# Optimization experiments

Measured on AMD Instinct MI355X. Metric: run time of the kernel, lower is better.

Reference implementation:

```python
import jax, jax.numpy as jnp
import numpy as np

B, S, ENC, DEC, ATT = 32, 2048, 1024, 1024, 1024


def setup_inputs() -> dict:
    key = jax.random.key(0)
    k1, k2, k3, k4, k5, k6 = jax.random.split(key, 6)
    sc = lambda fan_in: 1.0 / np.sqrt(fan_in)
    return {
        "encoder_hidden_states": jax.random.normal(k1, (B, S, ENC), dtype=jnp.float32),
        "decoder_hidden_state": jax.random.normal(k2, (B, 1, DEC), dtype=jnp.float32),
        # nn.Linear stores weight as [out, in]; we keep [in, out] for x @ W
        "U_a": jax.random.uniform(k3, (ENC, ATT), jnp.float32, -sc(ENC), sc(ENC)),
        "W_a": jax.random.uniform(k4, (DEC, ATT), jnp.float32, -sc(DEC), sc(DEC)),
        "v_t": jax.random.uniform(k5, (ATT, 1), jnp.float32, -sc(ATT), sc(ATT)),
        "ffn": jax.random.uniform(k6, (ENC + DEC, DEC), jnp.float32, -sc(ENC + DEC), sc(ENC + DEC)),
    }


def reference(encoder_hidden_states, decoder_hidden_state, U_a, W_a, v_t, ffn):
    # additive (Bahdanau) attention
    u = jnp.einsum('bse,ea->bsa', encoder_hidden_states, U_a)      # [B,S,A]
    w = jnp.einsum('bqd,da->bqa', decoder_hidden_state, W_a)       # [B,1,A]
    e = jnp.tanh(w + u) @ v_t                                      # [B,S,1]
    align = jax.nn.softmax(e, axis=1)                              # softmax over seq
    # context = alignment^T @ encoder_states  -> [B,1,E]
    context = jnp.einsum('bsq,bse->bqe', align, encoder_hidden_states)
    cat = jnp.concatenate([decoder_hidden_state, context], axis=-1)  # [B,1,D+E]
    output = jnp.tanh(cat @ ffn)                                     # [B,1,D]
    return (output, context)
```

## Files before the change

kernel.cpp:

```cpp
#include <hip/hip_runtime.h>
#include <hip/hip_bf16.h>
#include <cstdint>
#include <cstddef>

#define B_  32
#define S_  2048
#define E_  1024
#define A_  1024
#define D_  1024
#define M_TOT (B_ * S_)

typedef __attribute__((ext_vector_type(8))) __bf16 bf16x8;
typedef __attribute__((ext_vector_type(4))) float  f32x4;

__device__ __forceinline__ float fast_tanh(float x) {
    float cx = fminf(fmaxf(x, -15.f), 15.f);
    float e2 = __expf(2.f * cx);
    return 1.f - 2.f / (e2 + 1.f);
}

__device__ __forceinline__ bf16x8 pack8(float4 f0, float4 f1) {
    bf16x8 r;
    r[0] = (__bf16)f0.x; r[1] = (__bf16)f0.y; r[2] = (__bf16)f0.z; r[3] = (__bf16)f0.w;
    r[4] = (__bf16)f1.x; r[5] = (__bf16)f1.y; r[6] = (__bf16)f1.z; r[7] = (__bf16)f1.w;
    return r;
}

typedef __attribute__((address_space(3))) uint32_t lds_u32_t;
typedef __attribute__((address_space(1))) const uint32_t gbl_u32_t;
__device__ __forceinline__ void async_ld16(const void* g, void* l) {
    __builtin_amdgcn_global_load_lds((gbl_u32_t*)g,
                                     (lds_u32_t*)(uint32_t)(uintptr_t)l,
                                     16, 0, 0);
}

__global__ __launch_bounds__(256) void k_cvt(const float* __restrict__ enc,
                                             __bf16* __restrict__ encB) {
    size_t base = (size_t)blockIdx.x * 8192 + (size_t)threadIdx.x * 8;
    #pragma unroll
    for (int it = 0; it < 4; ++it) {
        size_t idx = base + (size_t)it * 2048;
        float4 f0 = *(const float4*)(enc + idx);
        float4 f1 = *(const float4*)(enc + idx + 4);
        *(bf16x8*)(encB + idx) = pack8(f0, f1);
    }
}

__global__ __launch_bounds__(256) void k_trans_U(const float* __restrict__ Ua,
                                                 __bf16* __restrict__ Ut) {
    __shared__ float tile[64][65];
    int bid = blockIdx.x;
    int k0 = (bid >> 4) * 64, n0 = (bid & 15) * 64;
    int t = threadIdx.x;
    int r = t >> 6, c = t & 63;
    #pragma unroll
    for (int i = 0; i < 16; ++i)
        tile[i * 4 + r][c] = Ua[(size_t)(k0 + i * 4 + r) * 1024 + n0 + c];
    __syncthreads();
    #pragma unroll
    for (int i = 0; i < 16; ++i)
        Ut[(size_t)(n0 + i * 4 + r) * 1024 + k0 + c] = (__bf16)tile[c][i * 4 + r];
}

__global__ __launch_bounds__(256) void k_w_part(const float* __restrict__ dec,
                                                const float* __restrict__ Wa,
                                                float* __restrict__ w_part) {
    int bid = blockIdx.x;
    int ac = bid & 3, b = (bid >> 2) & 31, kc = bid >> 7;
    int a = ac * 256 + threadIdx.x;
    int k0 = kc * 128;
    float acc = 0.f;
    #pragma unroll 8
    for (int k = 0; k < 128; ++k)
        acc += dec[b * 1024 + k0 + k] * Wa[(size_t)(k0 + k) * 1024 + a];
    w_part[kc * 32768 + b * 1024 + a] = acc;
}

template<bool ASYNC_A>
__global__ __launch_bounds__(256) void k_gemm_e(
        const float* __restrict__ enc, const __bf16* __restrict__ encB,
        const __bf16* __restrict__ Ut,
        const float* __restrict__ w_part, const float* __restrict__ v,
        float* __restrict__ e_part) {
    __shared__ __bf16 lX[2][128 * 32];
    __shared__ __bf16 lU[2][128 * 32];
    __shared__ float  e_lds[2][128];

    const int t = threadIdx.x;
    const int bid = blockIdx.x;
    const int xcd = bid & 7;
    const int j_  = bid >> 3;
    const int m_tile = xcd * 64 + (j_ >> 3);
    const int n_tile = j_ & 7;
    const int m0 = m_tile * 128;
    const int n0 = n_tile * 128;
    const int wave = t >> 6;
    const int lane = t & 63;
    const int q = lane >> 4;
    const int c = lane & 15;
    const int wm = (wave >> 1) * 64;
    const int wn = (wave & 1) * 64;

    f32x4 acc[4][4];
    #pragma unroll
    for (int i = 0; i < 4; ++i)
        #pragma unroll
        for (int j = 0; j < 4; ++j)
            #pragma unroll
            for (int r = 0; r < 4; ++r) acc[i][j][r] = 0.f;

    const int lrow = lane >> 2;
    const int p    = lane & 3;
    const int sw   = (lrow >> 1) & 3;
    const int lcolS = ((p ^ sw)) * 8;

    const int xrow = wave * 32;

    const float*  gxa = enc  + (size_t)(m0 + xrow + lrow) * 1024 + lcolS;
    const __bf16* gxb = encB + (size_t)(m0 + xrow + lrow) * 1024 + lcolS;
    const __bf16* gub = Ut   + (size_t)(n0 + xrow + lrow) * 1024 + lcolS;

    float4 f0, f1, f2, f3;
    auto loadA = [&](int kk) {
        const float* pp = gxa + kk;
        f0 = *(const float4*)pp;
        f1 = *(const float4*)(pp + 4);
        f2 = *(const float4*)(pp + 16 * 1024);
        f3 = *(const float4*)(pp + 16 * 1024 + 4);
    };
    auto writeA = [&](int bsel) {
        *(bf16x8*)(&lX[bsel][(xrow + lrow) * 32 + p * 8])      = pack8(f0, f1);
        *(bf16x8*)(&lX[bsel][(xrow + 16 + lrow) * 32 + p * 8]) = pack8(f2, f3);
    };
    auto stageA = [&](int kk, int bsel) {
        async_ld16(gxb + kk,             &lX[bsel][xrow * 32]);
        async_ld16(gxb + kk + 16 * 1024, &lX[bsel][(xrow + 16) * 32]);
    };
    auto stageB = [&](int kk, int bsel) {
        async_ld16(gub + kk,             &lU[bsel][xrow * 32]);
        async_ld16(gub + kk + 16 * 1024, &lU[bsel][(xrow + 16) * 32]);
    };

    const int fcol = (q ^ ((c >> 1) & 3)) * 8;
    auto compute = [&](int bsel) {
        bf16x8 af[4], bfr[4];
        #pragma unroll
        for (int i = 0; i < 4; ++i)
            af[i] = *(const bf16x8*)(&lX[bsel][(wm + i * 16 + c) * 32 + fcol]);
        #pragma unroll
        for (int j = 0; j < 4; ++j)
            bfr[j] = *(const bf16x8*)(&lU[bsel][(wn + j * 16 + c) * 32 + fcol]);
        #pragma unroll
        for (int i = 0; i < 4; ++i)
            #pragma unroll
            for (int j = 0; j < 4; ++j)
                acc[i][j] = __builtin_amdgcn_mfma_f32_16x16x32_bf16(af[i], bfr[j], acc[i][j], 0, 0, 0);
    };

    if constexpr (ASYNC_A) {
        stageA(0, 0); stageB(0, 0);
        __syncthreads();
        for (int kk = 0; kk < 1024; kk += 64) {
            if (kk + 32 < 1024) { stageA(kk + 32, 1); stageB(kk + 32, 1); }
            compute(0);
            __syncthreads();
            if (kk + 64 < 1024) { stageA(kk + 64, 0); stageB(kk + 64, 0); }
            compute(1);
            __syncthreads();
        }
    } else {
        loadA(0);
        stageB(0, 0);
        writeA(0);
        __syncthreads();
        for (int kk = 0; kk < 1024; kk += 64) {
            if (kk + 32 < 1024) { loadA(kk + 32); stageB(kk + 32, 1); }
            compute(0);
            if (kk + 32 < 1024) writeA(1);
            __syncthreads();
            if (kk + 64 < 1024) { loadA(kk + 64); stageB(kk + 64, 0); }
            compute(1);
            if (kk + 64 < 1024) writeA(0);
            __syncthreads();
        }
    }

    const int b_idx = m0 >> 11;
    float wv[4], vv[4];
    #pragma unroll
    for (int j = 0; j < 4; ++j) {
        int col = n0 + wn + j * 16 + c;
        float s = 0.f;
        #pragma unroll
        for (int pp = 0; pp < 8; ++pp) s += w_part[pp * 32768 + b_idx * 1024 + col];
        wv[j] = s;
        vv[j] = v[col];
    }
    #pragma unroll
    for (int i = 0; i < 4; ++i) {
        float s0 = 0.f, s1 = 0.f, s2 = 0.f, s3 = 0.f;
        #pragma unroll
        for (int j = 0; j < 4; ++j) {
            s0 += fast_tanh(wv[j] + acc[i][j][0]) * vv[j];
            s1 += fast_tanh(wv[j] + acc[i][j][1]) * vv[j];
            s2 += fast_tanh(wv[j] + acc[i][j][2]) * vv[j];
            s3 += fast_tanh(wv[j] + acc[i][j][3]) * vv[j];
        }
        #pragma unroll
        for (int off = 1; off < 16; off <<= 1) {
            s0 += __shfl_xor(s0, off, 16);
            s1 += __shfl_xor(s1, off, 16);
            s2 += __shfl_xor(s2, off, 16);
            s3 += __shfl_xor(s3, off, 16);
        }
        if (c == 0) {
            int row = wm + i * 16 + q * 4;
            e_lds[wave & 1][row + 0] = s0;
            e_lds[wave & 1][row + 1] = s1;
            e_lds[wave & 1][row + 2] = s2;
            e_lds[wave & 1][row + 3] = s3;
        }
    }
    __syncthreads();
    if (t < 128)
        e_part[(size_t)n_tile * M_TOT + m0 + t] = e_lds[0][t] + e_lds[1][t];
}

__global__ __launch_bounds__(256) void k_softmax(const float* __restrict__ ep,
                                                 float* __restrict__ al) {
    int b = blockIdx.x, t = threadIdx.x;
    float ev[8];
    #pragma unroll
    for (int i = 0; i < 8; ++i) {
        int s = i * 256 + t;
        float x = 0.f;
        #pragma unroll
        for (int p = 0; p < 8; ++p) x += ep[p * M_TOT + b * 2048 + s];
        ev[i] = x;
    }
    float mx = ev[0];
    #pragma unroll
    for (int i = 1; i < 8; ++i) mx = fmaxf(mx, ev[i]);
    #pragma unroll
    for (int off = 1; off < 64; off <<= 1) mx = fmaxf(mx, __shfl_xor(mx, off, 64));
    __shared__ float redm[4];
    if ((t & 63) == 0) redm[t >> 6] = mx;
    __syncthreads();
    mx = fmaxf(fmaxf(redm[0], redm[1]), fmaxf(redm[2], redm[3]));

    float ex[8], sm = 0.f;
    #pragma unroll
    for (int i = 0; i < 8; ++i) { ex[i] = __expf(ev[i] - mx); sm += ex[i]; }
    #pragma unroll
    for (int off = 1; off < 64; off <<= 1) sm += __shfl_xor(sm, off, 64);
    __shared__ float reds[4];
    if ((t & 63) == 0) reds[t >> 6] = sm;
    __syncthreads();
    sm = reds[0] + reds[1] + reds[2] + reds[3];
    float inv = 1.f / sm;
    #pragma unroll
    for (int i = 0; i < 8; ++i) al[b * 2048 + i * 256 + t] = ex[i] * inv;
}

__global__ __launch_bounds__(256) void k_ctx(const float* __restrict__ enc,
                                             const float* __restrict__ al,
                                             float* __restrict__ ctx_part) {
    int b  = blockIdx.x >> 5;
    int sc = blockIdx.x & 31;
    int t  = threadIdx.x;
    int e4 = t * 4;
    float ax = 0.f, ay = 0.f, az = 0.f, aw = 0.f;
    int sbase = sc * 64;
    for (int i = 0; i < 64; i += 4) {
        #pragma unroll
        for (int u = 0; u < 4; ++u) {
            int s = sbase + i + u;
            float a = al[b * 2048 + s];
            float4 x = *(const float4*)(enc + (size_t)(b * 2048 + s) * 1024 + e4);
            ax += a * x.x; ay += a * x.y; az += a * x.z; aw += a * x.w;
        }
    }
    float4 r; r.x = ax; r.y = ay; r.z = az; r.w = aw;
    *(float4*)(ctx_part + ((size_t)sc * 32 + b) * 1024 + e4) = r;
}

__global__ __launch_bounds__(256) void k_final(const float* __restrict__ dec,
                                               const float* __restrict__ ffn,
                                               const float* __restrict__ ctx_part,
                                               float* __restrict__ out) {
    int b  = blockIdx.x >> 4;
    int dc = blockIdx.x & 15;
    int t  = threadIdx.x;
    __shared__ float cat[2048];
    __shared__ float red[4][64];

    #pragma unroll
    for (int r = 0; r < 4; ++r) {
        int e = r * 256 + t;
        cat[e] = dec[b * 1024 + e];
        float s = 0.f;
        #pragma unroll
        for (int p = 0; p < 32; ++p) s += ctx_part[((size_t)p * 32 + b) * 1024 + e];
        cat[1024 + e] = s;
        if (dc == 0) out[32768 + b * 1024 + e] = s;
    }
    __syncthreads();

    int dl = t & 63, ic = t >> 6;
    int d  = dc * 64 + dl;
    float acc = 0.f;
    int i0 = ic * 512;
    for (int i = 0; i < 512; i += 4) {
        float4 cv = *(const float4*)(cat + i0 + i);
        const float* fr = ffn + (size_t)(i0 + i) * 1024 + d;
        acc += cv.x * fr[0];
        acc += cv.y * fr[1024];
        acc += cv.z * fr[2048];
        acc += cv.w * fr[3072];
    }
    red[ic][dl] = acc;
    __syncthreads();
    if (t < 64) {
        float s = red[0][t] + red[1][t] + red[2][t] + red[3][t];
        out[b * 1024 + dc * 64 + t] = fast_tanh(s);
    }
}

extern "C" void kernel_launch(void* const* d_in, const int* in_sizes, int n_in,
                              void* d_out, int out_size, void* d_ws, size_t ws_size,
                              hipStream_t stream) {
    const float* enc = (const float*)d_in[0];
    const float* dec = (const float*)d_in[1];
    const float* Ua  = (const float*)d_in[2];
    const float* Wa  = (const float*)d_in[3];
    const float* vt  = (const float*)d_in[4];
    const float* ffn = (const float*)d_in[5];
    float* out = (float*)d_out;

    char* ws = (char*)d_ws;
    size_t off = 0;
    __bf16* Ut       = (__bf16*)(ws + off); off += (size_t)A_ * E_ * 2;
    float*  e_part   = (float*)(ws + off);  off += (size_t)8 * M_TOT * 4;
    float*  al       = (float*)(ws + off);  off += (size_t)M_TOT * 4;
    float*  w_part   = (float*)(ws + off);  off += (size_t)8 * B_ * 1024 * 4;
    float*  ctx_part = (float*)(ws + off);  off += (size_t)32 * B_ * 1024 * 4;
    __bf16* encB     = (__bf16*)(ws + off); off += (size_t)M_TOT * E_ * 2;
    const bool use_async = ws_size >= off;

    k_trans_U<<<256, 256, 0, stream>>>(Ua, Ut);
    k_w_part<<<1024, 256, 0, stream>>>(dec, Wa, w_part);
    if (use_async) {
        k_cvt<<<8192, 256, 0, stream>>>(enc, encB);
        k_gemm_e<true><<<4096, 256, 0, stream>>>(enc, encB, Ut, w_part, vt, e_part);
    } else {
        k_gemm_e<false><<<4096, 256, 0, stream>>>(enc, encB, Ut, w_part, vt, e_part);
    }
    k_softmax<<<B_, 256, 0, stream>>>(e_part, al);
    k_ctx<<<B_ * 32, 256, 0, stream>>>(enc, al, ctx_part);
    k_final<<<B_ * 16, 256, 0, stream>>>(dec, ffn, ctx_part, out);
}
```

Before: 696.9 us.

## Replace 128x128 bf16 GEMM with 256x256 8-wave ping-pong MFMA kernel

The main energy GEMM now uses a 256x256 output tile per 512-thread block with 64-wide K steps, an XOR-swizzled LDS layout and double-buffered async global-to-LDS loads. Its schedule interleaves LDS reads, MFMA quadrants raised with s_setprio, and prefetches, all separated by explicit barriers and vmcnt waits. Larger tiles halve the number of N partials, so softmax now sums 4 partials instead of 8. The aim is higher arithmetic intensity and better overlap of memory with MFMA, at the cost of more registers and LDS per block and a hand-written wait schedule that is fragile.

```diff
diff --git a/kernel.cpp b/kernel.cpp
--- a/kernel.cpp
+++ b/kernel.cpp
@@ -76,10 +76,152 @@
     w_part[kc * 32768 + b * 1024 + a] = acc;
 }
 
-template<bool ASYNC_A>
-__global__ __launch_bounds__(256) void k_gemm_e(
-        const float* __restrict__ enc, const __bf16* __restrict__ encB,
-        const __bf16* __restrict__ Ut,
+#define PBAR  __builtin_amdgcn_s_barrier()
+#define LGKM0 asm volatile("s_waitcnt lgkmcnt(0)" ::: "memory")
+
+#define DS_A(mh) do { \
+    _Pragma("unroll") for (int mf = 0; mf < 4; ++mf) \
+        _Pragma("unroll") for (int k2 = 0; k2 < 2; ++k2) \
+            a[mf][k2] = *(const bf16x8*)&L[buf][0][(wm + (mh)*64 + mf*16 + c)*64 + (((k2*4 + q) ^ (c & 7)))*8]; \
+} while (0)
+
+#define DS_B(nh, bb) do { \
+    _Pragma("unroll") for (int nf = 0; nf < 2; ++nf) \
+        _Pragma("unroll") for (int k2 = 0; k2 < 2; ++k2) \
+            bb[nf][k2] = *(const bf16x8*)&L[buf][1][(wn + (nh)*32 + nf*16 + c)*64 + (((k2*4 + q) ^ (c & 7)))*8]; \
+} while (0)
+
+#define MMA_Q(mh, nh, bb) do { \
+    __builtin_amdgcn_s_setprio(1); \
+    _Pragma("unroll") for (int mf = 0; mf < 4; ++mf) \
+        _Pragma("unroll") for (int nf = 0; nf < 2; ++nf) \
+            _Pragma("unroll") for (int k2 = 0; k2 < 2; ++k2) \
+                acc[(mh)*4 + mf][(nh)*2 + nf] = __builtin_amdgcn_mfma_f32_16x16x32_bf16( \
+                    a[mf][k2], bb[nf][k2], acc[(mh)*4 + mf][(nh)*2 + nf], 0, 0, 0); \
+    __builtin_amdgcn_s_setprio(0); \
+} while (0)
+
+__global__ __launch_bounds__(512, 2) void k_gemm8(
+        const __bf16* __restrict__ encB, const __bf16* __restrict__ Ut,
+        const float* __restrict__ w_part, const float* __restrict__ v,
+        float* __restrict__ e_part) {
+    __shared__ __bf16 L[2][2][16384];
+
+    const int t = threadIdx.x;
+    const int wid = t >> 6, lane = t & 63;
+    const int q = lane >> 4, c = lane & 15;
+    const int wm = (wid >> 2) * 128;
+    const int wn = (wid & 3) * 64;
+
+    const int p = blockIdx.x;
+    const int xcd = p & 7, j = p >> 3;
+    const int m_tile = xcd * 32 + (j >> 2);
+    const int n_tile = j & 3;
+    const int m0 = m_tile * 256, n0 = n_tile * 256;
+
+    const int scol = ((lane & 7) ^ (lane >> 3)) * 8;
+    const __bf16* gA = encB + (size_t)(m0 + (t >> 3)) * 1024 + scol;
+    const __bf16* gB = Ut   + (size_t)(n0 + (t >> 3)) * 1024 + scol;
+    const int ldsoff0 = wid * 512;
+
+    auto stage = [&](int kind, int h, int kt2) {
+        const __bf16* src = (kind ? gB : gA) + (size_t)h * 128 * 1024 + (size_t)kt2 * 64;
+        __bf16* dst = &L[kt2 & 1][kind][h * 8192 + ldsoff0];
+        async_ld16(src,             dst);
+        async_ld16(src + 64 * 1024, dst + 4096);
+    };
+
+    f32x4 acc[8][4];
+    #pragma unroll
+    for (int i = 0; i < 8; ++i)
+        #pragma unroll
+        for (int jj = 0; jj < 4; ++jj)
+            #pragma unroll
+            for (int r = 0; r < 4; ++r) acc[i][jj][r] = 0.f;
+
+    bf16x8 a[4][2], b0[2][2], b1[2][2];
+
+    stage(0, 0, 0); stage(1, 0, 0); stage(0, 1, 0); stage(1, 1, 0);
+    stage(0, 0, 1); stage(1, 0, 1);
+    asm volatile("s_waitcnt vmcnt(4)" ::: "memory");
+    PBAR;
+    __builtin_amdgcn_sched_barrier(0);
+
+    #pragma unroll 2
+    for (int kt = 0; kt < 16; ++kt) {
+        const int buf = kt & 1;
+        DS_A(0);
+        DS_B(0, b0);
+        if (kt < 15) { stage(0, 1, kt + 1); stage(1, 1, kt + 1); }
+        PBAR; LGKM0;
+        MMA_Q(0, 0, b0);
+        PBAR;
+        DS_B(1, b1);
+        PBAR; LGKM0;
+        MMA_Q(0, 1, b1);
+        PBAR;
+        DS_A(1);
+        PBAR; LGKM0;
+        MMA_Q(1, 1, b1);
+        PBAR;
+        if (kt < 14) { stage(0, 0, kt + 2); stage(1, 0, kt + 2); }
+        PBAR;
+        MMA_Q(1, 0, b0);
+        if (kt < 15) {
+            if (kt < 14) asm volatile("s_waitcnt vmcnt(4)" ::: "memory");
+            else         asm volatile("s_waitcnt vmcnt(0)" ::: "memory");
+            PBAR;
+            __builtin_amdgcn_sched_barrier(0);
+        }
+    }
+
+    __syncthreads();
+    float* e_red = (float*)&L[0][0][0];
+
+    const int b_idx = m0 >> 11;
+    float wv[4], vv[4];
+    #pragma unroll
+    for (int nf = 0; nf < 4; ++nf) {
+        int col = n0 + wn + nf * 16 + c;
+        float s = 0.f;
+        #pragma unroll
+        for (int pp = 0; pp < 8; ++pp) s += w_part[pp * 32768 + b_idx * 1024 + col];
+        wv[nf] = s;
+        vv[nf] = v[col];
+    }
+    #pragma unroll
+    for (int mf = 0; mf < 8; ++mf) {
+        float s0 = 0.f, s1 = 0.f, s2 = 0.f, s3 = 0.f;
+        #pragma unroll
+        for (int nf = 0; nf < 4; ++nf) {
+            s0 += fast_tanh(wv[nf] + acc[mf][nf][0]) * vv[nf];
+            s1 += fast_tanh(wv[nf] + acc[mf][nf][1]) * vv[nf];
+            s2 += fast_tanh(wv[nf] + acc[mf][nf][2]) * vv[nf];
+            s3 += fast_tanh(wv[nf] + acc[mf][nf][3]) * vv[nf];
+        }
+        #pragma unroll
+        for (int off = 1; off < 16; off <<= 1) {
+            s0 += __shfl_xor(s0, off, 16);
+            s1 += __shfl_xor(s1, off, 16);
+            s2 += __shfl_xor(s2, off, 16);
+            s3 += __shfl_xor(s3, off, 16);
+        }
+        if (c == 0) {
+            int row = wm + mf * 16 + q * 4;
+            e_red[(wid & 3) * 256 + row + 0] = s0;
+            e_red[(wid & 3) * 256 + row + 1] = s1;
+            e_red[(wid & 3) * 256 + row + 2] = s2;
+            e_red[(wid & 3) * 256 + row + 3] = s3;
+        }
+    }
+    __syncthreads();
+    if (t < 256)
+        e_part[(size_t)n_tile * M_TOT + m0 + t] =
+            e_red[t] + e_red[256 + t] + e_red[512 + t] + e_red[768 + t];
+}
+
+__global__ __launch_bounds__(256) void k_gemm_fb(
+        const float* __restrict__ enc, const __bf16* __restrict__ Ut,
         const float* __restrict__ w_part, const float* __restrict__ v,
         float* __restrict__ e_part) {
     __shared__ __bf16 lX[2][128 * 32];
@@ -113,12 +255,10 @@
     const int p    = lane & 3;
     const int sw   = (lrow >> 1) & 3;
     const int lcolS = ((p ^ sw)) * 8;
-
     const int xrow = wave * 32;
 
-    const float*  gxa = enc  + (size_t)(m0 + xrow + lrow) * 1024 + lcolS;
-    const __bf16* gxb = encB + (size_t)(m0 + xrow + lrow) * 1024 + lcolS;
-    const __bf16* gub = Ut   + (size_t)(n0 + xrow + lrow) * 1024 + lcolS;
+    const float*  gxa = enc + (size_t)(m0 + xrow + lrow) * 1024 + lcolS;
+    const __bf16* gub = Ut  + (size_t)(n0 + xrow + lrow) * 1024 + lcolS;
 
     float4 f0, f1, f2, f3;
     auto loadA = [&](int kk) {
@@ -132,15 +272,10 @@
         *(bf16x8*)(&lX[bsel][(xrow + lrow) * 32 + p * 8])      = pack8(f0, f1);
         *(bf16x8*)(&lX[bsel][(xrow + 16 + lrow) * 32 + p * 8]) = pack8(f2, f3);
     };
-    auto stageA = [&](int kk, int bsel) {
-        async_ld16(gxb + kk,             &lX[bsel][xrow * 32]);
-        async_ld16(gxb + kk + 16 * 1024, &lX[bsel][(xrow + 16) * 32]);
-    };
     auto stageB = [&](int kk, int bsel) {
         async_ld16(gub + kk,             &lU[bsel][xrow * 32]);
         async_ld16(gub + kk + 16 * 1024, &lU[bsel][(xrow + 16) * 32]);
     };
-
     const int fcol = (q ^ ((c >> 1) & 3)) * 8;
     auto compute = [&](int bsel) {
         bf16x8 af[4], bfr[4];
@@ -157,32 +292,19 @@
                 acc[i][j] = __builtin_amdgcn_mfma_f32_16x16x32_bf16(af[i], bfr[j], acc[i][j], 0, 0, 0);
     };
 
-    if constexpr (ASYNC_A) {
-        stageA(0, 0); stageB(0, 0);
+    loadA(0);
+    stageB(0, 0);
+    writeA(0);
+    __syncthreads();
+    for (int kk = 0; kk < 1024; kk += 64) {
+        if (kk + 32 < 1024) { loadA(kk + 32); stageB(kk + 32, 1); }
+        compute(0);
+        if (kk + 32 < 1024) writeA(1);
         __syncthreads();
-        for (int kk = 0; kk < 1024; kk += 64) {
-            if (kk + 32 < 1024) { stageA(kk + 32, 1); stageB(kk + 32, 1); }
-            compute(0);
-            __syncthreads();
-            if (kk + 64 < 1024) { stageA(kk + 64, 0); stageB(kk + 64, 0); }
-            compute(1);
-            __syncthreads();
-        }
-    } else {
-        loadA(0);
-        stageB(0, 0);
-        writeA(0);
+        if (kk + 64 < 1024) { loadA(kk + 64); stageB(kk + 64, 0); }
+        compute(1);
+        if (kk + 64 < 1024) writeA(0);
         __syncthreads();
-        for (int kk = 0; kk < 1024; kk += 64) {
-            if (kk + 32 < 1024) { loadA(kk + 32); stageB(kk + 32, 1); }
-            compute(0);
-            if (kk + 32 < 1024) writeA(1);
-            __syncthreads();
-            if (kk + 64 < 1024) { loadA(kk + 64); stageB(kk + 64, 0); }
-            compute(1);
-            if (kk + 64 < 1024) writeA(0);
-            __syncthreads();
-        }
     }
 
     const int b_idx = m0 >> 11;
@@ -226,6 +348,7 @@
         e_part[(size_t)n_tile * M_TOT + m0 + t] = e_lds[0][t] + e_lds[1][t];
 }
 
+template<int NP>
 __global__ __launch_bounds__(256) void k_softmax(const float* __restrict__ ep,
                                                  float* __restrict__ al) {
     int b = blockIdx.x, t = threadIdx.x;
@@ -235,7 +358,7 @@
         int s = i * 256 + t;
         float x = 0.f;
         #pragma unroll
-        for (int p = 0; p < 8; ++p) x += ep[p * M_TOT + b * 2048 + s];
+        for (int p = 0; p < NP; ++p) x += ep[p * M_TOT + b * 2048 + s];
         ev[i] = x;
     }
     float mx = ev[0];
@@ -351,11 +474,12 @@
     k_w_part<<<1024, 256, 0, stream>>>(dec, Wa, w_part);
     if (use_async) {
         k_cvt<<<8192, 256, 0, stream>>>(enc, encB);
-        k_gemm_e<true><<<4096, 256, 0, stream>>>(enc, encB, Ut, w_part, vt, e_part);
+        k_gemm8<<<1024, 512, 0, stream>>>(encB, Ut, w_part, vt, e_part);
+        k_softmax<4><<<B_, 256, 0, stream>>>(e_part, al);
     } else {
-        k_gemm_e<false><<<4096, 256, 0, stream>>>(enc, encB, Ut, w_part, vt, e_part);
-    }
-    k_softmax<<<B_, 256, 0, stream>>>(e_part, al);
+        k_gemm_fb<<<4096, 256, 0, stream>>>(enc, Ut, w_part, vt, e_part);
+        k_softmax<8><<<B_, 256, 0, stream>>>(e_part, al);
+    }
     k_ctx<<<B_ * 32, 256, 0, stream>>>(enc, al, ctx_part);
     k_final<<<B_ * 16, 256, 0, stream>>>(dec, ffn, ctx_part, out);
 }
```

Result: faster. 631.8 us (-9.3%).
